# Performance work log

Hardware: AMD Instinct MI355X
Metric: run time of the kernel (lower is better)

## Reference

```python
import jax, jax.numpy as jnp
import numpy as np

D_MODEL = 1024
NHEAD = 16
HEAD_DIM = D_MODEL // NHEAD
B, S = 8, 1024
NEG = -1e9  # finite stand-in for -inf (same softmax result, grad-safe)


def setup_inputs() -> dict:
    key = jax.random.key(0)
    ks = jax.random.split(key, 12)
    sc = 1.0 / np.sqrt(D_MODEL)
    inp = {
        "q": jax.random.normal(ks[0], (B, S, D_MODEL), jnp.float32),
        "k": jax.random.normal(ks[1], (B, S, D_MODEL), jnp.float32),
        "v": jax.random.normal(ks[2], (B, S, D_MODEL), jnp.float32),
        "padding_mask": jax.random.bernoulli(ks[3], 0.1, (B, S)),
        "causal_mask": jnp.where(jnp.tril(jnp.ones((S, S), bool)), 0.0, NEG).astype(jnp.float32),
        "wq": jax.random.normal(ks[4], (D_MODEL, D_MODEL), jnp.float32) * sc,
        "bq": jax.random.normal(ks[5], (D_MODEL,), jnp.float32) * sc,
        "wk": jax.random.normal(ks[6], (D_MODEL, D_MODEL), jnp.float32) * sc,
        "wv": jax.random.normal(ks[7], (D_MODEL, D_MODEL), jnp.float32) * sc,
        "bv": jax.random.normal(ks[8], (D_MODEL,), jnp.float32) * sc,
        "wo": jax.random.normal(ks[9], (D_MODEL, D_MODEL), jnp.float32) * sc,
        "bo": jax.random.normal(ks[10], (D_MODEL,), jnp.float32) * sc,
    }
    return inp


def reference(q, k, v, padding_mask, causal_mask, wq, bq, wk, wv, bv, wo, bo):
    b = q.shape[0]
    # projections (torch Linear: x @ W.T + b); k_linear has no bias
    qp = q @ wq.T + bq
    kp = k @ wk.T
    vp = v @ wv.T + bv
    # [B, S, H, Dh] -> [B, H, S, Dh]
    qh = qp.reshape(b, -1, NHEAD, HEAD_DIM).transpose(0, 2, 1, 3)
    kh = kp.reshape(b, -1, NHEAD, HEAD_DIM).transpose(0, 2, 1, 3)
    vh = vp.reshape(b, -1, NHEAD, HEAD_DIM).transpose(0, 2, 1, 3)
    scores = jnp.einsum("bhqd,bhkd->bhqk", qh, kh) / np.sqrt(HEAD_DIM).astype(np.float32)
    scores = jnp.where(padding_mask[:, None, None, :], NEG, scores)
    scores = scores + causal_mask[None, None, :, :]
    attn = jax.nn.softmax(scores, axis=-1)
    out = jnp.einsum("bhqk,bhkd->bhqd", attn, vh)
    out = out.transpose(0, 2, 1, 3).reshape(b, -1, D_MODEL)
    return out @ wo.T + bo
```

## Files before the change

kernel.cpp:

```cpp
#include <hip/hip_runtime.h>
#include <hip/hip_bf16.h>
#include <cstdint>
#include <math.h>


typedef __bf16 bf16_t;
typedef __bf16 bf16x8 __attribute__((ext_vector_type(8)));
typedef __bf16 bf16x4 __attribute__((ext_vector_type(4)));
typedef float  f32x4  __attribute__((ext_vector_type(4)));

#define MFMA16(a, b, c) __builtin_amdgcn_mfma_f32_16x16x32_bf16((a), (b), (c), 0, 0, 0)
#define NEGV (-1e9f)

__device__ __forceinline__ void gl_lds16(const void* gp, void* lp) {
  __builtin_amdgcn_global_load_lds(
      (__attribute__((address_space(1))) void*)(gp),
      (__attribute__((address_space(3))) void*)(lp), 16, 0, 0);
}

__device__ __forceinline__ void bar() {
  asm volatile("" ::: "memory");
  __builtin_amdgcn_s_barrier();
  asm volatile("" ::: "memory");
}

__device__ __forceinline__ unsigned int pk2(float lo, float hi) {
  unsigned short a = __builtin_bit_cast(unsigned short, (bf16_t)lo);
  unsigned short b = __builtin_bit_cast(unsigned short, (bf16_t)hi);
  return (unsigned int)a | ((unsigned int)b << 16);
}

__device__ __forceinline__ void cvt_body(const float* __restrict__ in,
                                         bf16_t* __restrict__ out, int i) {
  const float4* p = reinterpret_cast<const float4*>(in) + (size_t)i * 2;
  float4 a = p[0], b = p[1];
  bf16x8 r = {(bf16_t)a.x, (bf16_t)a.y, (bf16_t)a.z, (bf16_t)a.w,
              (bf16_t)b.x, (bf16_t)b.y, (bf16_t)b.z, (bf16_t)b.w};
  *reinterpret_cast<bf16x8*>(out + (size_t)i * 8) = r;
}

__global__ __launch_bounds__(256) void cvt_all(
    const float* __restrict__ q, const float* __restrict__ k, const float* __restrict__ v,
    const float* __restrict__ wq, const float* __restrict__ wk,
    const float* __restrict__ wv, const float* __restrict__ wo,
    bf16_t* __restrict__ oq, bf16_t* __restrict__ ok, bf16_t* __restrict__ ov,
    bf16_t* __restrict__ owq, bf16_t* __restrict__ owk,
    bf16_t* __restrict__ owv, bf16_t* __restrict__ owo) {
  const int bid = (int)blockIdx.x;
  if (bid < 12288) {
    const int s = bid >> 12;
    const int i = (bid & 4095) * 256 + (int)threadIdx.x;
    cvt_body(s == 0 ? q : (s == 1 ? k : v),
             s == 0 ? oq : (s == 1 ? ok : ov), i);
  } else {
    const int r = bid - 12288;
    const int s = r >> 9;
    const int i = (r & 511) * 256 + (int)threadIdx.x;
    cvt_body(s == 0 ? wq : (s == 1 ? wk : (s == 2 ? wv : wo)),
             s == 0 ? owq : (s == 1 ? owk : (s == 2 ? owv : owo)), i);
  }
}

__global__ __launch_bounds__(512, 4) void gemm_qkv(const bf16_t* __restrict__ qbf,
                                                   const bf16_t* __restrict__ kbf,
                                                   const bf16_t* __restrict__ vbf,
                                                   const bf16_t* __restrict__ wqb,
                                                   const bf16_t* __restrict__ wkb,
                                                   const bf16_t* __restrict__ wvb,
                                                   const float* __restrict__ bq,
                                                   const float* __restrict__ bv,
                                                   bf16_t* __restrict__ qp,
                                                   bf16_t* __restrict__ kp,
                                                   bf16_t* __restrict__ vtw) {
  __shared__ __align__(16) char lds[73728];
  const int bid = (int)blockIdx.x;
  const int z = bid >> 8;
  const int idx = bid & 255;
  const int p = ((idx >> 6) << 3) | (idx & 7);
  const int n = (idx >> 3) & 7;
  const bf16_t* A = z == 0 ? qbf : (z == 1 ? kbf : vbf);
  const bf16_t* W = z == 0 ? wqb : (z == 1 ? wkb : wvb);
  const int t = threadIdx.x;
  const int w = t >> 6, l = t & 63, lr = l & 15, lg = l >> 4;
  const int wr = w >> 1, wc = w & 1;
  const int m0 = p * 256, n0 = n * 128;
  const int K = 1024, N = 1024;

  const int gc = (t & 3) ^ ((t >> 3) & 3);
  const bf16_t* Ag = A + (size_t)(m0 + (t >> 2)) * K + gc * 8;
  const bf16_t* Wg = W + (size_t)(n0 + (t >> 2)) * K + gc * 8;

  auto stageA = [&](int buf, int tile) {
    char* dst = lds + buf * 16384 + t * 16;
    const size_t kt = (size_t)tile * 32;
    gl_lds16(Ag + kt,                   dst);
    gl_lds16(Ag + kt + (size_t)128 * K, dst + 8192);
  };
  auto stageB = [&](int buf, int tile) {
    gl_lds16(Wg + (size_t)tile * 32, lds + 49152 + buf * 8192 + t * 16);
  };

  stageA(0, 0); stageB(0, 0); stageA(1, 1); stageB(1, 1);
  asm volatile("s_waitcnt vmcnt(3)" ::: "memory");
  bar();

  f32x4 acc[4][4] = {};
  const int cofs = (lg ^ ((lr >> 1) & 3)) << 4;

  for (int T = 0; T < 32; ++T) {
    const int cur = T % 3;
    const char* Ab = lds + cur * 16384;
    const char* Bb = lds + 49152 + cur * 8192;
    bf16x8 af[4], bfr[4];
#pragma unroll
    for (int mt = 0; mt < 4; mt++)
      af[mt] = *(const bf16x8*)(Ab + (wr * 64 + mt * 16 + lr) * 64 + cofs);
#pragma unroll
    for (int nt = 0; nt < 4; nt++)
      bfr[nt] = *(const bf16x8*)(Bb + (wc * 64 + nt * 16 + lr) * 64 + cofs);
    if (T + 2 < 32) { stageA((T + 2) % 3, T + 2); stageB((T + 2) % 3, T + 2); }
    if (T < 30)       asm volatile("s_waitcnt vmcnt(3)" ::: "memory");
    else if (T == 30) asm volatile("s_waitcnt vmcnt(0)" ::: "memory");
    bar();
    asm volatile("s_waitcnt lgkmcnt(0)" ::: "memory");
    __builtin_amdgcn_s_setprio(1);
#pragma unroll
    for (int mt = 0; mt < 4; mt++)
#pragma unroll
      for (int nt = 0; nt < 4; nt++)
        acc[mt][nt] = MFMA16(af[mt], bfr[nt], acc[mt][nt]);
    __builtin_amdgcn_s_setprio(0);
    bar();
  }

  if (z != 2) {
    bf16_t* outp = (z == 0) ? qp : kp;
    const float sc = (z == 0) ? 0.125f : 1.0f;
#pragma unroll
    for (int nt = 0; nt < 4; nt++) {
      const int col = n0 + wc * 64 + nt * 16 + lr;
      const float bb = (z == 0) ? bq[col] : 0.0f;
#pragma unroll
      for (int mt = 0; mt < 4; mt++)
#pragma unroll
        for (int i = 0; i < 4; i++) {
          const int row = m0 + wr * 64 + mt * 16 + lg * 4 + i;
          outp[(size_t)row * N + col] = (bf16_t)((acc[mt][nt][i] + bb) * sc);
        }
    }
  } else {
    __syncthreads();
    char* Tl = lds;
#pragma unroll
    for (int nt = 0; nt < 4; nt++) {
      const int col_l = wc * 64 + nt * 16 + lr;
      const float bb = bv[n0 + col_l];
#pragma unroll
      for (int mt = 0; mt < 4; mt++)
#pragma unroll
        for (int i = 0; i < 4; i++) {
          const int row_l = wr * 64 + mt * 16 + lg * 4 + i;
          *(bf16_t*)(Tl + col_l * 512 + ((row_l * 2) ^ ((col_l & 7) << 4))) =
              (bf16_t)(acc[mt][nt][i] + bb);
        }
    }
    __syncthreads();
    const int b = m0 >> 10, s0 = m0 & 1023;
    const int c_l = t >> 2, sub = t & 3;
    bf16_t* dst = vtw + (size_t)(b * 1024 + n0 + c_l) * 1024 + s0 + sub * 64;
    const char* Trow = Tl + c_l * 512;
    const int sw2 = (c_l & 7) << 4;
#pragma unroll
    for (int jj = 0; jj < 8; jj++) {
      const int lc = sub * 8 + jj;
      bf16x8 vv = *(const bf16x8*)(Trow + ((lc << 4) ^ sw2));
      *(bf16x8*)(dst + jj * 8) = vv;
    }
  }
}

__global__ __launch_bounds__(256, 2) void gemm_out(const bf16_t* __restrict__ A,
                                                   const bf16_t* __restrict__ W,
                                                   const float* __restrict__ bias,
                                                   float* __restrict__ outp) {
  __shared__ __align__(16) char lds[49152];
  const int bid = (int)blockIdx.x;
  const int p = ((bid >> 6) << 3) | (bid & 7);
  const int n = (bid >> 3) & 7;
  const int t = threadIdx.x;
  const int w = t >> 6, l = t & 63, lr = l & 15, lg = l >> 4;
  const int wr = w >> 1, wc = w & 1;
  const int m0 = p * 128, n0 = n * 128;
  const int K = 1024, N = 1024;

  const int gc = (t & 3) ^ ((t >> 3) & 3);
  const bf16_t* Ag = A + (size_t)(m0 + (t >> 2)) * K + gc * 8;
  const bf16_t* Wg = W + (size_t)(n0 + (t >> 2)) * K + gc * 8;

  auto stageA = [&](int buf, int tile) {
    char* dst = lds + buf * 8192 + t * 16;
    const size_t kt = (size_t)tile * 32;
    gl_lds16(Ag + kt,                  dst);
    gl_lds16(Ag + kt + (size_t)64 * K, dst + 4096);
  };
  auto stageB = [&](int buf, int tile) {
    char* dst = lds + 24576 + buf * 8192 + t * 16;
    const size_t kt = (size_t)tile * 32;
    gl_lds16(Wg + kt,                  dst);
    gl_lds16(Wg + kt + (size_t)64 * K, dst + 4096);
  };

  stageA(0, 0); stageB(0, 0); stageA(1, 1); stageB(1, 1);
  asm volatile("s_waitcnt vmcnt(4)" ::: "memory");
  bar();

  f32x4 acc[4][4] = {};
  const int cofs = (lg ^ ((lr >> 1) & 3)) << 4;

  for (int T = 0; T < 32; ++T) {
    const int cur = T % 3;
    const char* Ab = lds + cur * 8192;
    const char* Bb = lds + 24576 + cur * 8192;
    bf16x8 af[4], bfr[4];
#pragma unroll
    for (int mt = 0; mt < 4; mt++)
      af[mt] = *(const bf16x8*)(Ab + (wr * 64 + mt * 16 + lr) * 64 + cofs);
#pragma unroll
    for (int nt = 0; nt < 4; nt++)
      bfr[nt] = *(const bf16x8*)(Bb + (wc * 64 + nt * 16 + lr) * 64 + cofs);
    if (T + 2 < 32) { stageA((T + 2) % 3, T + 2); stageB((T + 2) % 3, T + 2); }
    if (T < 30)       asm volatile("s_waitcnt vmcnt(4)" ::: "memory");
    else if (T == 30) asm volatile("s_waitcnt vmcnt(0)" ::: "memory");
    bar();
    asm volatile("s_waitcnt lgkmcnt(0)" ::: "memory");
    __builtin_amdgcn_s_setprio(1);
#pragma unroll
    for (int mt = 0; mt < 4; mt++)
#pragma unroll
      for (int nt = 0; nt < 4; nt++)
        acc[mt][nt] = MFMA16(af[mt], bfr[nt], acc[mt][nt]);
    __builtin_amdgcn_s_setprio(0);
    bar();
  }

#pragma unroll
  for (int nt = 0; nt < 4; nt++) {
    const int col = n0 + wc * 64 + nt * 16 + lr;
    const float bb = bias[col];
#pragma unroll
    for (int mt = 0; mt < 4; mt++)
#pragma unroll
      for (int i = 0; i < 4; i++) {
        const int row = m0 + wr * 64 + mt * 16 + lg * 4 + i;
        outp[(size_t)row * N + col] = acc[mt][nt][i] + bb;
      }
  }
}

__device__ __forceinline__ void pack_bfly(const f32x4 (&s)[4], int lg,
                                          bf16x8& pbv0, bf16x8& pbv1) {
  unsigned int u[4][2], sh[4][2];
#pragma unroll
  for (int nt = 0; nt < 4; nt++) {
    u[nt][0] = pk2(s[nt][0], s[nt][1]);
    u[nt][1] = pk2(s[nt][2], s[nt][3]);
  }
#pragma unroll
  for (int nt = 0; nt < 4; nt++) {
    sh[nt][0] = (unsigned int)__shfl_xor((int)u[nt][0], 16, 64);
    sh[nt][1] = (unsigned int)__shfl_xor((int)u[nt][1], 16, 64);
  }
  const bool ev = (lg & 1) == 0;
  unsigned int Y[8];
  Y[0] = ev ? u[0][0] : sh[1][0];  Y[1] = ev ? u[0][1] : sh[1][1];
  Y[2] = ev ? u[2][0] : sh[3][0];  Y[3] = ev ? u[2][1] : sh[3][1];
  Y[4] = ev ? sh[0][0] : u[1][0];  Y[5] = ev ? sh[0][1] : u[1][1];
  Y[6] = ev ? sh[2][0] : u[3][0];  Y[7] = ev ? sh[2][1] : u[3][1];
  const bool mid = (lg == 1) || (lg == 2);
#pragma unroll
  for (int j = 0; j < 8; j++) {
    const unsigned int z = (unsigned int)__shfl_xor((int)Y[j], 48, 64);
    Y[j] = mid ? z : Y[j];
  }
  union U8 { unsigned int u[4]; bf16x8 v; };
  U8 p0, p1;
  p0.u[0] = Y[0]; p0.u[1] = Y[1]; p0.u[2] = Y[4]; p0.u[3] = Y[5];
  p1.u[0] = Y[2]; p1.u[1] = Y[3]; p1.u[2] = Y[6]; p1.u[3] = Y[7];
  pbv0 = p0.v;
  pbv1 = p1.v;
}

__global__ __launch_bounds__(512, 8) void attn_fused(const bf16_t* __restrict__ qp,
                                                     const bf16_t* __restrict__ kp,
                                                     const bf16_t* __restrict__ vt,
                                                     const int* __restrict__ pad,
                                                     bf16_t* __restrict__ outp) {
  __shared__ bf16_t Ks[2][64 * 64];
  __shared__ bf16_t Vts[2][64 * 64];
  __shared__ int padI[1024];
  __shared__ int sfl[8], sfh[8];
  const int t = threadIdx.x, w = t >> 6, l = t & 63, lr = l & 15, lg = l >> 4;
  const int L = (int)blockIdx.x;
  const int bh = (L & 7) + ((L >> 6) << 3);
  const int j = (L >> 3) & 7;
  const int b = bh >> 4, h = bh & 15;
  const int lo = j, hi = 15 - j;

  const int srow = t >> 3, sc = t & 7;
  const int gc = sc ^ (srow & 7);
  const bf16_t* kgb = kp + (size_t)(b * 1024 + srow) * 1024 + h * 64 + gc * 8;
  const bf16_t* vgb = vt + (size_t)(bh * 64 + srow) * 1024 + gc * 8;

  auto stage = [&](int bufi, int k0s) {
    gl_lds16(kgb + (size_t)k0s * 1024, (char*)(Ks[bufi]) + t * 16);
    gl_lds16(vgb + k0s,                (char*)(Vts[bufi]) + t * 16);
  };

  bool unl = false, unh = false;
  for (int jj = t; jj <= hi * 64; jj += 512) {
    const bool u = (pad[b * 1024 + jj] == 0);
    unh |= u;
    unl |= (u && (jj <= lo * 64));
  }
  const bool al = __any(unl), ah = __any(unh);
  if (l == 0) { sfl[w] = al ? 1 : 0; sfh[w] = ah ? 1 : 0; }

  stage(0, 0);
  if (t < 256) gl_lds16(pad + b * 1024 + t * 4, (char*)padI + t * 16);

  const int mytile = (w < 4) ? hi : lo;
  const int qrow_l = mytile * 64 + (w & 3) * 16 + lr;
  const int base16 = mytile * 64 + (w & 3) * 16;
  const bf16_t* qg = qp + (size_t)(b * 1024 + qrow_l) * 1024 + h * 64 + lg * 8;
  const bf16x8 qa0 = *reinterpret_cast<const bf16x8*>(qg);
  const bf16x8 qa1 = *reinterpret_cast<const bf16x8*>(qg + 32);

  __syncthreads();
  int ul = 0, uh = 0;
#pragma unroll
  for (int i = 0; i < 8; i++) { ul |= sfl[i]; uh |= sfh[i]; }
  const bool mydeg = (w < 4) ? (uh == 0) : (ul == 0);
  const int ktEnd = (ul == 0) ? 16 : (hi + 1);

  f32x4 o[4] = {};
  float m_ = -INFINITY, ld_ = 0.0f;

  for (int kt = 0; kt < ktEnd; ++kt) {
    const int cur = kt & 1;
    if (kt + 1 < ktEnd) {
      stage(cur ^ 1, (kt + 1) * 64);
      asm volatile("s_waitcnt vmcnt(2)" ::: "memory");
    } else {
      asm volatile("s_waitcnt vmcnt(0)" ::: "memory");
    }
    __builtin_amdgcn_s_barrier();

    if (kt <= mytile || mydeg) {
      const char* Kb = (const char*)(Ks[cur]);
      const char* Vb = (const char*)(Vts[cur]);
      const int k0 = kt * 64;

      f32x4 s[4] = {};
      __builtin_amdgcn_s_setprio(1);
#pragma unroll
      for (int nt = 0; nt < 4; nt++) {
        const int row = nt * 16 + lr;
        const int sw = (row & 7) << 4;
        bf16x8 kb0 = *reinterpret_cast<const bf16x8*>(Kb + row * 128 + ((lg * 16) ^ sw));
        bf16x8 kb1 = *reinterpret_cast<const bf16x8*>(Kb + row * 128 + ((lg * 16 + 64) ^ sw));
        s[nt] = MFMA16(kb0, qa0, s[nt]);
        s[nt] = MFMA16(kb1, qa1, s[nt]);
      }
      __builtin_amdgcn_s_setprio(0);

      const bool nc = (k0 + 63 > base16);
#pragma unroll
      for (int nt = 0; nt < 4; nt++) {
        const int kc4 = k0 + nt * 16 + lg * 4;
        const int4 pd = *reinterpret_cast<const int4*>(&padI[kc4]);
        const int pdv[4] = {pd.x, pd.y, pd.z, pd.w};
#pragma unroll
        for (int i = 0; i < 4; i++) {
          float v = s[nt][i];
          if (pdv[i]) v = NEGV;
          if (nc && (kc4 + i > qrow_l)) v += NEGV;
          s[nt][i] = v;
        }
      }

      float mx = s[0][0];
#pragma unroll
      for (int nt = 0; nt < 4; nt++)
#pragma unroll
        for (int i = 0; i < 4; i++) mx = fmaxf(mx, s[nt][i]);
      mx = fmaxf(mx, __shfl_xor(mx, 16, 64));
      mx = fmaxf(mx, __shfl_xor(mx, 32, 64));

      if (!__all(mx <= m_ - 88.0f)) {
        if (!__all(mx <= m_ + 8.0f)) {
          const float mn = fmaxf(m_, mx);
          const float scl = __expf(m_ - mn);
          m_ = mn;
          ld_ *= scl;
#pragma unroll
          for (int nt = 0; nt < 4; nt++) o[nt] *= scl;
        }
        float a = 0.0f;
#pragma unroll
        for (int nt = 0; nt < 4; nt++)
#pragma unroll
          for (int i = 0; i < 4; i++) {
            const float p = __expf(s[nt][i] - m_);
            s[nt][i] = p;
            a += p;
          }
        a += __shfl_xor(a, 16, 64);
        a += __shfl_xor(a, 32, 64);
        ld_ += a;

        bf16x8 pb0, pb1;
        pack_bfly(s, lg, pb0, pb1);

        __builtin_amdgcn_s_setprio(1);
#pragma unroll
        for (int nt = 0; nt < 4; nt++) {
          const int vrow = nt * 16 + lr;
          const int vsw = (vrow & 7) << 4;
          bf16x8 vf0 = *reinterpret_cast<const bf16x8*>(Vb + vrow * 128 + ((lg * 16) ^ vsw));
          bf16x8 vf1 = *reinterpret_cast<const bf16x8*>(Vb + vrow * 128 + ((64 + lg * 16) ^ vsw));
          o[nt] = MFMA16(vf0, pb0, o[nt]);
          o[nt] = MFMA16(vf1, pb1, o[nt]);
        }
        __builtin_amdgcn_s_setprio(0);
      }
    }
    __builtin_amdgcn_s_barrier();
  }

  const float rinv = 1.0f / ld_;
#pragma unroll
  for (int nt = 0; nt < 4; nt++) {
    bf16x4 rr = {(bf16_t)(o[nt][0] * rinv), (bf16_t)(o[nt][1] * rinv),
                 (bf16_t)(o[nt][2] * rinv), (bf16_t)(o[nt][3] * rinv)};
    *reinterpret_cast<bf16x4*>(outp + (size_t)(b * 1024 + qrow_l) * 1024 + h * 64 + nt * 16 + lg * 4) = rr;
  }
}

extern "C" void kernel_launch(void* const* d_in, const int* in_sizes, int n_in,
                              void* d_out, int out_size, void* d_ws, size_t ws_size,
                              hipStream_t stream) {
  const float* q   = (const float*)d_in[0];
  const float* k   = (const float*)d_in[1];
  const float* v   = (const float*)d_in[2];
  const int*   pad = (const int*)d_in[3];
  const float* wq  = (const float*)d_in[5];
  const float* bq  = (const float*)d_in[6];
  const float* wk  = (const float*)d_in[7];
  const float* wv  = (const float*)d_in[8];
  const float* bv  = (const float*)d_in[9];
  const float* wo  = (const float*)d_in[10];
  const float* bo  = (const float*)d_in[11];

  char* ws = (char*)d_ws;
  const size_t MiB = 1024 * 1024;
  bf16_t* qbf = (bf16_t*)(ws + 0 * MiB);
  bf16_t* kbf = (bf16_t*)(ws + 16 * MiB);
  bf16_t* vbf = (bf16_t*)(ws + 32 * MiB);
  bf16_t* qp  = (bf16_t*)(ws + 48 * MiB);
  bf16_t* kp  = (bf16_t*)(ws + 64 * MiB);
  bf16_t* vtw = (bf16_t*)(ws + 80 * MiB);
  bf16_t* wqb = (bf16_t*)(ws + 96 * MiB);
  bf16_t* wkb = (bf16_t*)(ws + 98 * MiB);
  bf16_t* wvb = (bf16_t*)(ws + 100 * MiB);
  bf16_t* wob = (bf16_t*)(ws + 102 * MiB);
  bf16_t* attnO = qbf;

  cvt_all<<<14336, 256, 0, stream>>>(q, k, v, wq, wk, wv, wo,
                                     qbf, kbf, vbf, wqb, wkb, wvb, wob);

  gemm_qkv<<<768, 512, 0, stream>>>(qbf, kbf, vbf, wqb, wkb, wvb, bq, bv, qp, kp, vtw);

  attn_fused<<<1024, 512, 0, stream>>>(qp, kp, vtw, pad, attnO);

  gemm_out<<<512, 256, 0, stream>>>(attnO, wob, bo, (float*)d_out);
}
```

Measured before the change: 171.2 us.

## Fuse fp32-to-bf16 activation conversion into QKV GEMM operand loading

Activations q, k and v are no longer converted to bf16 by a separate pass. The QKV GEMM now streams fp32 tiles straight into LDS and converts them to bf16 in registers right before the MFMA. This removes a full read and write of the 96 MiB activation tensors plus their later bf16 reread. In exchange, the GEMM tile is reshaped to 128x128 with 256 threads and twice as many blocks, and the A operand moves twice the bytes per K step, with conversion work repeated across the 8 N-tiles.

```diff
diff --git a/kernel.cpp b/kernel.cpp
--- a/kernel.cpp
+++ b/kernel.cpp
@@ -39,31 +39,21 @@
   *reinterpret_cast<bf16x8*>(out + (size_t)i * 8) = r;
 }
 
-__global__ __launch_bounds__(256) void cvt_all(
-    const float* __restrict__ q, const float* __restrict__ k, const float* __restrict__ v,
+__global__ __launch_bounds__(256) void cvt_w(
     const float* __restrict__ wq, const float* __restrict__ wk,
     const float* __restrict__ wv, const float* __restrict__ wo,
-    bf16_t* __restrict__ oq, bf16_t* __restrict__ ok, bf16_t* __restrict__ ov,
     bf16_t* __restrict__ owq, bf16_t* __restrict__ owk,
     bf16_t* __restrict__ owv, bf16_t* __restrict__ owo) {
   const int bid = (int)blockIdx.x;
-  if (bid < 12288) {
-    const int s = bid >> 12;
-    const int i = (bid & 4095) * 256 + (int)threadIdx.x;
-    cvt_body(s == 0 ? q : (s == 1 ? k : v),
-             s == 0 ? oq : (s == 1 ? ok : ov), i);
-  } else {
-    const int r = bid - 12288;
-    const int s = r >> 9;
-    const int i = (r & 511) * 256 + (int)threadIdx.x;
-    cvt_body(s == 0 ? wq : (s == 1 ? wk : (s == 2 ? wv : wo)),
-             s == 0 ? owq : (s == 1 ? owk : (s == 2 ? owv : owo)), i);
-  }
-}
-
-__global__ __launch_bounds__(512, 4) void gemm_qkv(const bf16_t* __restrict__ qbf,
-                                                   const bf16_t* __restrict__ kbf,
-                                                   const bf16_t* __restrict__ vbf,
+  const int s = bid >> 9;
+  const int i = (bid & 511) * 256 + (int)threadIdx.x;
+  cvt_body(s == 0 ? wq : (s == 1 ? wk : (s == 2 ? wv : wo)),
+           s == 0 ? owq : (s == 1 ? owk : (s == 2 ? owv : owo)), i);
+}
+
+__global__ __launch_bounds__(256, 2) void gemm_qkv(const float* __restrict__ qf,
+                                                   const float* __restrict__ kf,
+                                                   const float* __restrict__ vf,
                                                    const bf16_t* __restrict__ wqb,
                                                    const bf16_t* __restrict__ wkb,
                                                    const bf16_t* __restrict__ wvb,
@@ -74,38 +64,43 @@
                                                    bf16_t* __restrict__ vtw) {
   __shared__ __align__(16) char lds[73728];
   const int bid = (int)blockIdx.x;
-  const int z = bid >> 8;
-  const int idx = bid & 255;
+  const int z = bid >> 9;
+  const int idx = bid & 511;
   const int p = ((idx >> 6) << 3) | (idx & 7);
   const int n = (idx >> 3) & 7;
-  const bf16_t* A = z == 0 ? qbf : (z == 1 ? kbf : vbf);
+  const float*  A = z == 0 ? qf : (z == 1 ? kf : vf);
   const bf16_t* W = z == 0 ? wqb : (z == 1 ? wkb : wvb);
   const int t = threadIdx.x;
   const int w = t >> 6, l = t & 63, lr = l & 15, lg = l >> 4;
   const int wr = w >> 1, wc = w & 1;
-  const int m0 = p * 256, n0 = n * 128;
+  const int m0 = p * 128, n0 = n * 128;
   const int K = 1024, N = 1024;
 
-  const int gc = (t & 3) ^ ((t >> 3) & 3);
-  const bf16_t* Ag = A + (size_t)(m0 + (t >> 2)) * K + gc * 8;
-  const bf16_t* Wg = W + (size_t)(n0 + (t >> 2)) * K + gc * 8;
+  const int gcA = (t & 7) ^ ((t >> 3) & 7);
+  const float* Ag = A + (size_t)(m0 + (t >> 3)) * K + gcA * 4;
+  const int gcB = (t & 3) ^ ((t >> 3) & 3);
+  const bf16_t* Wg = W + (size_t)(n0 + (t >> 2)) * K + gcB * 8;
 
   auto stageA = [&](int buf, int tile) {
     char* dst = lds + buf * 16384 + t * 16;
     const size_t kt = (size_t)tile * 32;
-    gl_lds16(Ag + kt,                   dst);
-    gl_lds16(Ag + kt + (size_t)128 * K, dst + 8192);
+#pragma unroll
+    for (int c = 0; c < 4; c++)
+      gl_lds16(Ag + (size_t)(c * 32) * K + kt, dst + c * 4096);
   };
   auto stageB = [&](int buf, int tile) {
-    gl_lds16(Wg + (size_t)tile * 32, lds + 49152 + buf * 8192 + t * 16);
+    char* dst = lds + 49152 + buf * 8192 + t * 16;
+    const size_t kt = (size_t)tile * 32;
+    gl_lds16(Wg + kt,                  dst);
+    gl_lds16(Wg + kt + (size_t)64 * K, dst + 4096);
   };
 
   stageA(0, 0); stageB(0, 0); stageA(1, 1); stageB(1, 1);
-  asm volatile("s_waitcnt vmcnt(3)" ::: "memory");
+  asm volatile("s_waitcnt vmcnt(6)" ::: "memory");
   bar();
 
   f32x4 acc[4][4] = {};
-  const int cofs = (lg ^ ((lr >> 1) & 3)) << 4;
+  const int cofsB = (lg ^ ((lr >> 1) & 3)) << 4;
 
   for (int T = 0; T < 32; ++T) {
     const int cur = T % 3;
@@ -113,13 +108,19 @@
     const char* Bb = lds + 49152 + cur * 8192;
     bf16x8 af[4], bfr[4];
 #pragma unroll
-    for (int mt = 0; mt < 4; mt++)
-      af[mt] = *(const bf16x8*)(Ab + (wr * 64 + mt * 16 + lr) * 64 + cofs);
+    for (int mt = 0; mt < 4; mt++) {
+      const int R = wr * 64 + mt * 16 + lr;
+      const int sw = R & 7;
+      f32x4 a0 = *(const f32x4*)(Ab + R * 128 + (((2 * lg) ^ sw) << 4));
+      f32x4 a1 = *(const f32x4*)(Ab + R * 128 + (((2 * lg + 1) ^ sw) << 4));
+      af[mt] = (bf16x8){(bf16_t)a0[0], (bf16_t)a0[1], (bf16_t)a0[2], (bf16_t)a0[3],
+                        (bf16_t)a1[0], (bf16_t)a1[1], (bf16_t)a1[2], (bf16_t)a1[3]};
+    }
 #pragma unroll
     for (int nt = 0; nt < 4; nt++)
-      bfr[nt] = *(const bf16x8*)(Bb + (wc * 64 + nt * 16 + lr) * 64 + cofs);
+      bfr[nt] = *(const bf16x8*)(Bb + (wc * 64 + nt * 16 + lr) * 64 + cofsB);
     if (T + 2 < 32) { stageA((T + 2) % 3, T + 2); stageB((T + 2) % 3, T + 2); }
-    if (T < 30)       asm volatile("s_waitcnt vmcnt(3)" ::: "memory");
+    if (T < 30)       asm volatile("s_waitcnt vmcnt(6)" ::: "memory");
     else if (T == 30) asm volatile("s_waitcnt vmcnt(0)" ::: "memory");
     bar();
     asm volatile("s_waitcnt lgkmcnt(0)" ::: "memory");
@@ -160,20 +161,20 @@
 #pragma unroll
         for (int i = 0; i < 4; i++) {
           const int row_l = wr * 64 + mt * 16 + lg * 4 + i;
-          *(bf16_t*)(Tl + col_l * 512 + ((row_l * 2) ^ ((col_l & 7) << 4))) =
+          *(bf16_t*)(Tl + col_l * 256 + ((row_l * 2) ^ ((col_l & 7) << 4))) =
               (bf16_t)(acc[mt][nt][i] + bb);
         }
     }
     __syncthreads();
     const int b = m0 >> 10, s0 = m0 & 1023;
-    const int c_l = t >> 2, sub = t & 3;
-    bf16_t* dst = vtw + (size_t)(b * 1024 + n0 + c_l) * 1024 + s0 + sub * 64;
-    const char* Trow = Tl + c_l * 512;
-    const int sw2 = (c_l & 7) << 4;
+    const int c_l = t >> 1, half = t & 1;
+    bf16_t* dst = vtw + (size_t)(b * 1024 + n0 + c_l) * 1024 + s0 + half * 64;
+    const char* Trow = Tl + c_l * 256;
+    const int sw = c_l & 7;
 #pragma unroll
     for (int jj = 0; jj < 8; jj++) {
-      const int lc = sub * 8 + jj;
-      bf16x8 vv = *(const bf16x8*)(Trow + ((lc << 4) ^ sw2));
+      const int lc = half * 8 + jj;
+      bf16x8 vv = *(const bf16x8*)(Trow + ((lc ^ sw) << 4));
       *(bf16x8*)(dst + jj * 8) = vv;
     }
   }
@@ -463,9 +464,7 @@
 
   char* ws = (char*)d_ws;
   const size_t MiB = 1024 * 1024;
-  bf16_t* qbf = (bf16_t*)(ws + 0 * MiB);
-  bf16_t* kbf = (bf16_t*)(ws + 16 * MiB);
-  bf16_t* vbf = (bf16_t*)(ws + 32 * MiB);
+  bf16_t* attnO = (bf16_t*)(ws + 0 * MiB);
   bf16_t* qp  = (bf16_t*)(ws + 48 * MiB);
   bf16_t* kp  = (bf16_t*)(ws + 64 * MiB);
   bf16_t* vtw = (bf16_t*)(ws + 80 * MiB);
@@ -473,12 +472,10 @@
   bf16_t* wkb = (bf16_t*)(ws + 98 * MiB);
   bf16_t* wvb = (bf16_t*)(ws + 100 * MiB);
   bf16_t* wob = (bf16_t*)(ws + 102 * MiB);
-  bf16_t* attnO = qbf;
-
-  cvt_all<<<14336, 256, 0, stream>>>(q, k, v, wq, wk, wv, wo,
-                                     qbf, kbf, vbf, wqb, wkb, wvb, wob);
-
-  gemm_qkv<<<768, 512, 0, stream>>>(qbf, kbf, vbf, wqb, wkb, wvb, bq, bv, qp, kp, vtw);
+
+  cvt_w<<<2048, 256, 0, stream>>>(wq, wk, wv, wo, wqb, wkb, wvb, wob);
+
+  gemm_qkv<<<1536, 256, 0, stream>>>(q, k, v, wqb, wkb, wvb, bq, bv, qp, kp, vtw);
 
   attn_fused<<<1024, 512, 0, stream>>>(qp, kp, vtw, pad, attnO);
 
```

After: 167.4 us. 2.2% less time.
